# Kernel tuning notes

Hardware: AMD Instinct MI355X
Metric: run time of the kernel (lower is better)

## Reference

```python
import jax, jax.numpy as jnp
import numpy as np

B, L, E, H, FF = 2, 2048, 1024, 16, 4096
DH = E // H
EPS = 1e-5
# NOTE: source has attn_scale = 1 / dh**(-0.5) == sqrt(dh) (multiplies, not divides)
ATTN_SCALE = float(DH) ** 0.5


def _layernorm(x, w, b):
    mu = jnp.mean(x, axis=-1, keepdims=True)
    var = jnp.mean((x - mu) ** 2, axis=-1, keepdims=True)
    return (x - mu) * jax.lax.rsqrt(var + EPS) * w + b


def setup_inputs() -> dict:
    key = jax.random.key(0)
    ks = jax.random.split(key, 8)
    s = 0.02
    return {
        "x": jax.random.normal(ks[0], (B, L, E), jnp.float32),
        "ln1_w": jnp.ones((E,), jnp.float32),
        "ln1_b": jnp.zeros((E,), jnp.float32),
        "wq": jax.random.normal(ks[1], (E, E), jnp.float32) * s,
        "bq": jnp.zeros((E,), jnp.float32),
        "wk": jax.random.normal(ks[2], (E, E), jnp.float32) * s,
        "bk": jnp.zeros((E,), jnp.float32),
        "wv": jax.random.normal(ks[3], (E, E), jnp.float32) * s,
        "bv": jnp.zeros((E,), jnp.float32),
        "wo": jax.random.normal(ks[4], (E, E), jnp.float32) * s,
        "bo": jnp.zeros((E,), jnp.float32),
        "ln2_w": jnp.ones((E,), jnp.float32),
        "ln2_b": jnp.zeros((E,), jnp.float32),
        "wu": jax.random.normal(ks[5], (E, FF), jnp.float32) * s,
        "bu": jnp.zeros((FF,), jnp.float32),
        "wd": jax.random.normal(ks[6], (FF, E), jnp.float32) * s,
        "bd": jnp.zeros((E,), jnp.float32),
    }


def reference(x, ln1_w, ln1_b, wq, bq, wk, bk, wv, bv, wo, bo,
              ln2_w, ln2_b, wu, bu, wd, bd):
    # --- attention block (pre-LN, manual softmax attention) ---
    xn = _layernorm(x, ln1_w, ln1_b)                       # [B,L,E]
    q = (xn @ wq + bq).reshape(B, L, H, DH)
    k = (xn @ wk + bk).reshape(B, L, H, DH)
    v = (xn @ wv + bv).reshape(B, L, H, DH)
    score = jnp.einsum("blhd,bmhd->bhlm", q, k) * ATTN_SCALE  # [B,H,L,L]
    attn = jax.nn.softmax(score, axis=-1)
    ctx = jnp.einsum("bhlm,bmhd->blhd", attn, v).reshape(B, L, E)
    hidden = x + (ctx @ wo + bo)
    # --- FFN block (pre-LN, GELU) ---
    hn = _layernorm(hidden, ln2_w, ln2_b)
    up = jax.nn.gelu(hn @ wu + bu, approximate=False)      # [B,L,F]
    down = up @ wd + bd
    return hidden + down
```

## Files before the change

### kernel.cpp

```cpp
#include <hip/hip_runtime.h>
#include <stdint.h>


typedef __attribute__((ext_vector_type(8))) short short8;
typedef __attribute__((ext_vector_type(4))) float floatx4;
typedef __attribute__((ext_vector_type(16))) float floatx16;

extern "C" __device__ float __ocml_native_exp2_f32(float);
#define EXP2(x) __ocml_native_exp2_f32(x)

#define MFMA_BF16(a, b, c) __builtin_amdgcn_mfma_f32_16x16x32_bf16((a), (b), (c), 0, 0, 0)
#define MFMA32(a, b, c) __builtin_amdgcn_mfma_f32_32x32x16_bf16((a), (b), (c), 0, 0, 0)

__device__ __forceinline__ unsigned short f2bf(float f) {
  union { float f; unsigned int u; } v; v.f = f;
  unsigned int r = v.u + 0x7FFFu + ((v.u >> 16) & 1u);
  return (unsigned short)(r >> 16);
}

__device__ __forceinline__ unsigned int f2u(float f) {
  union { float f; unsigned int u; } v; v.f = f; return v.u;
}

__device__ __forceinline__ short8 pack4(unsigned a, unsigned b, unsigned c, unsigned d) {
  union { unsigned u[4]; short8 s; } v;
  v.u[0] = a; v.u[1] = b; v.u[2] = c; v.u[3] = d;
  return v.s;
}

__device__ __forceinline__ void gl_lds16(const unsigned short* g, unsigned short* l) {
  __builtin_amdgcn_global_load_lds(
      (const __attribute__((address_space(1))) unsigned int*)g,
      (__attribute__((address_space(3))) unsigned int*)l, 16, 0, 0);
}

template <int MODE, int BN>
__global__ __launch_bounds__(256)
void gemm_bt(const unsigned short* __restrict__ A,
             const unsigned short* __restrict__ Bt,
             const float* __restrict__ bias,
             void* __restrict__ outp,
             const float* __restrict__ res,
             int K,
             void* __restrict__ out2, void* __restrict__ out3,
             const float* __restrict__ bias2, const float* __restrict__ bias3) {
  constexpr int BM = 128, BK = 64;
  constexpr int MI = (BN == 128) ? 4 : 2;
  constexpr int NI = 4;
  __shared__ __align__(16) unsigned short As[BM * BK];
  __shared__ __align__(16) unsigned short Bs[BN * BK];
  const int tid = threadIdx.x;
  const int wave = tid >> 6, lane = tid & 63, l16 = lane & 15, quad = lane >> 4;
  const int m0 = blockIdx.y * BM, n0 = blockIdx.x * BN;
  const int wm = (BN == 128) ? (wave >> 1) * 64 : wave * 32;
  const int wn = (BN == 128) ? (wave & 1) * 64 : 0;
  const int sw = l16 & 7;
  const int sl0 = (quad ^ sw) << 3;
  const int sl1 = sl0 ^ 32;

  floatx4 acc[MI][NI] = {};

  for (int k0 = 0; k0 < K; k0 += BK) {
    __syncthreads();
#pragma unroll
    for (int c = 0; c < (BM * BK) / 2048; ++c) {
      const int e = (c * 256 + tid) * 8;
      const int row = e >> 6, c8 = (e >> 3) & 7;
      gl_lds16(A + (size_t)(m0 + row) * K + k0 + ((c8 ^ (row & 7)) << 3), &As[e]);
    }
#pragma unroll
    for (int c = 0; c < (BN * BK) / 2048; ++c) {
      const int e = (c * 256 + tid) * 8;
      const int row = e >> 6, c8 = (e >> 3) & 7;
      gl_lds16(Bt + (size_t)(n0 + row) * K + k0 + ((c8 ^ (row & 7)) << 3), &Bs[e]);
    }
    __syncthreads();

    short8 af0[MI], af1[MI], bf0[NI], bf1[NI];
#pragma unroll
    for (int i = 0; i < MI; ++i) {
      af0[i] = *(const short8*)&As[(wm + i * 16 + l16) * BK + sl0];
      af1[i] = *(const short8*)&As[(wm + i * 16 + l16) * BK + sl1];
    }
#pragma unroll
    for (int i = 0; i < NI; ++i) {
      bf0[i] = *(const short8*)&Bs[(wn + i * 16 + l16) * BK + sl0];
      bf1[i] = *(const short8*)&Bs[(wn + i * 16 + l16) * BK + sl1];
    }
    __builtin_amdgcn_sched_barrier(0);
#pragma unroll
    for (int mi = 0; mi < MI; ++mi)
#pragma unroll
      for (int ni = 0; ni < NI; ++ni) {
        acc[mi][ni] = MFMA_BF16(af0[mi], bf0[ni], acc[mi][ni]);
        acc[mi][ni] = MFMA_BF16(af1[mi], bf1[ni], acc[mi][ni]);
      }
  }

  const int seg = (MODE == 0) ? (n0 >> 10) : 0;
  const float* bptr = bias;
  if constexpr (MODE == 0) bptr = (seg == 0) ? bias : (seg == 1 ? bias2 : bias3);

  float bcol[NI];
#pragma unroll
  for (int ni = 0; ni < NI; ++ni) {
    const int n = n0 + wn + ni * 16 + l16;
    bcol[ni] = bptr[(MODE == 0) ? (n & 1023) : n];
  }

#pragma unroll
  for (int mi = 0; mi < MI; ++mi) {
#pragma unroll
    for (int r = 0; r < 4; ++r) {
      const int m = m0 + wm + mi * 16 + quad * 4 + r;
#pragma unroll
      for (int ni = 0; ni < NI; ++ni) {
        const int n = n0 + wn + ni * 16 + l16;
        const float c = acc[mi][ni][r] + bcol[ni];
        if constexpr (MODE == 0) {
          const int b_ = m >> 11, l = m & 2047, hd = n & 1023;
          const size_t idx =
              ((size_t)((b_ * 16 + (hd >> 6)) * 2048 + l)) * 64 + (hd & 63);
          if (seg == 0)       ((unsigned short*)outp)[idx] = f2bf(c * 11.5415603270f);
          else if (seg == 1)  ((unsigned short*)out2)[idx] = f2bf(c);
          else                ((unsigned short*)out3)[idx] = f2bf(c);
        } else if constexpr (MODE == 1) {
          ((float*)outp)[(size_t)m * 1024 + n] = res[(size_t)m * 1024 + n] + c;
        } else if constexpr (MODE == 2) {
          const float g = 0.5f * c * (1.0f + erff(c * 0.70710678118654752f));
          ((unsigned short*)outp)[(size_t)m * 4096 + n] = f2bf(g);
        } else {
          ((float*)outp)[(size_t)m * 1024 + n] = res[(size_t)m * 1024 + n] + c;
        }
      }
    }
  }
}

__device__ __forceinline__ void stage_p3(const unsigned short* __restrict__ A,
                                         const unsigned short* __restrict__ Bt,
                                         int K, int m0, int n0, int k0, int tid,
                                         unsigned short* Asb, unsigned short* Bsb) {
#pragma unroll
  for (int c = 0; c < 4; ++c) {
    const int e = (c * 256 + tid) * 8;
    const int row = e >> 6, c8 = (e >> 3) & 7;
    gl_lds16(A + (size_t)(m0 + row) * K + k0 + ((c8 ^ (row & 7)) << 3), Asb + e);
  }
#pragma unroll
  for (int c = 0; c < 2; ++c) {
    const int e = (c * 256 + tid) * 8;
    const int row = e >> 6, c8 = (e >> 3) & 7;
    gl_lds16(Bt + (size_t)(n0 + row) * K + k0 + ((c8 ^ (row & 7)) << 3), Bsb + e);
  }
}

__global__ __launch_bounds__(256)
void gemm_bt_p3(const unsigned short* __restrict__ A,
                const unsigned short* __restrict__ Bt,
                const float* __restrict__ bias,
                float* __restrict__ outp,
                const float* __restrict__ res,
                int K) {
  constexpr int BM = 128, BN = 64, BK = 64, MI = 2, NI = 4;
  __shared__ __align__(16) unsigned short As[3][BM * BK];
  __shared__ __align__(16) unsigned short Bs[3][BN * BK];
  const int tid = threadIdx.x;
  const int wave = tid >> 6, lane = tid & 63, l16 = lane & 15, quad = lane >> 4;
  const int m0 = blockIdx.y * BM, n0 = blockIdx.x * BN;
  const int wm = wave * 32;
  const int sw = l16 & 7;
  const int sl0 = (quad ^ sw) << 3;
  const int sl1 = sl0 ^ 32;

  floatx4 acc[MI][NI] = {};

  const int nt = K / BK;
  stage_p3(A, Bt, K, m0, n0, 0 * BK, tid, As[0], Bs[0]);
  stage_p3(A, Bt, K, m0, n0, 1 * BK, tid, As[1], Bs[1]);
  stage_p3(A, Bt, K, m0, n0, 2 * BK, tid, As[2], Bs[2]);

  for (int t = 0; t < nt; ++t) {
    if (t < nt - 2)       asm volatile("s_waitcnt vmcnt(12)" ::: "memory");
    else if (t == nt - 2) asm volatile("s_waitcnt vmcnt(6)" ::: "memory");
    else                  asm volatile("s_waitcnt vmcnt(0)" ::: "memory");
    __builtin_amdgcn_s_barrier();

    const unsigned short* Ab = As[t % 3];
    const unsigned short* Bb = Bs[t % 3];
    short8 af0[MI], af1[MI], bf0[NI], bf1[NI];
#pragma unroll
    for (int i = 0; i < MI; ++i) {
      af0[i] = *(const short8*)&Ab[(wm + i * 16 + l16) * BK + sl0];
      af1[i] = *(const short8*)&Ab[(wm + i * 16 + l16) * BK + sl1];
    }
#pragma unroll
    for (int i = 0; i < NI; ++i) {
      bf0[i] = *(const short8*)&Bb[(i * 16 + l16) * BK + sl0];
      bf1[i] = *(const short8*)&Bb[(i * 16 + l16) * BK + sl1];
    }
#pragma unroll
    for (int mi = 0; mi < MI; ++mi)
#pragma unroll
      for (int ni = 0; ni < NI; ++ni) {
        acc[mi][ni] = MFMA_BF16(af0[mi], bf0[ni], acc[mi][ni]);
        acc[mi][ni] = MFMA_BF16(af1[mi], bf1[ni], acc[mi][ni]);
      }

    __builtin_amdgcn_s_barrier();
    if (t + 3 < nt)
      stage_p3(A, Bt, K, m0, n0, (t + 3) * BK, tid, As[t % 3], Bs[t % 3]);
  }

  float bcol[NI];
#pragma unroll
  for (int ni = 0; ni < NI; ++ni) bcol[ni] = bias[n0 + ni * 16 + l16];

#pragma unroll
  for (int mi = 0; mi < MI; ++mi) {
#pragma unroll
    for (int r = 0; r < 4; ++r) {
      const int m = m0 + wm + mi * 16 + quad * 4 + r;
#pragma unroll
      for (int ni = 0; ni < NI; ++ni) {
        const int n = n0 + ni * 16 + l16;
        const float c = acc[mi][ni][r] + bcol[ni];
        outp[(size_t)m * 1024 + n] = res[(size_t)m * 1024 + n] + c;
      }
    }
  }
}

__global__ __launch_bounds__(256)
void layernorm_kernel(const float* __restrict__ x, const float* __restrict__ w,
                      const float* __restrict__ b, unsigned short* __restrict__ out) {
  const int row = blockIdx.x, tid = threadIdx.x;
  const int wave = tid >> 6, lane = tid & 63;
  const float4 v = ((const float4*)(x + (size_t)row * 1024))[tid];
  float s = v.x + v.y + v.z + v.w;
  float s2 = v.x * v.x + v.y * v.y + v.z * v.z + v.w * v.w;
#pragma unroll
  for (int off = 32; off > 0; off >>= 1) {
    s += __shfl_down(s, off);
    s2 += __shfl_down(s2, off);
  }
  __shared__ float red[8];
  if (lane == 0) { red[wave] = s; red[4 + wave] = s2; }
  __syncthreads();
  const float ts = red[0] + red[1] + red[2] + red[3];
  const float ts2 = red[4] + red[5] + red[6] + red[7];
  const float mu = ts * (1.0f / 1024.0f);
  const float var = ts2 * (1.0f / 1024.0f) - mu * mu;
  const float rs = rsqrtf(var + 1e-5f);
  const float4 wv = ((const float4*)w)[tid];
  const float4 bv = ((const float4*)b)[tid];
  ushort4 o;
  o.x = f2bf((v.x - mu) * rs * wv.x + bv.x);
  o.y = f2bf((v.y - mu) * rs * wv.y + bv.y);
  o.z = f2bf((v.z - mu) * rs * wv.z + bv.z);
  o.w = f2bf((v.w - mu) * rs * wv.w + bv.w);
  ((ushort4*)(out + (size_t)row * 1024))[tid] = o;
}

__global__ __launch_bounds__(256)
void transpose_cast4(const float* __restrict__ s0, const float* __restrict__ s1,
                     const float* __restrict__ s2, const float* __restrict__ s3,
                     unsigned short* __restrict__ dst) {
  __shared__ float tile[32][33];
  const int z = blockIdx.z;
  const float* in = (z == 0) ? s0 : (z == 1) ? s1 : (z == 2) ? s2 : s3;
  unsigned short* out = dst + (size_t)z * 1024 * 1024;
  const int tx = threadIdx.x, ty = threadIdx.y;
  const int c0 = blockIdx.x * 32, r0 = blockIdx.y * 32;
#pragma unroll
  for (int i = 0; i < 4; ++i)
    tile[ty + 8 * i][tx] = in[(size_t)(r0 + ty + 8 * i) * 1024 + c0 + tx];
  __syncthreads();
#pragma unroll
  for (int i = 0; i < 4; ++i)
    out[(size_t)(c0 + ty + 8 * i) * 1024 + r0 + tx] = f2bf(tile[tx][ty + 8 * i]);
}

__global__ __launch_bounds__(256)
void transpose_cast(const float* __restrict__ in, unsigned short* __restrict__ out,
                    int R, int C) {
  __shared__ float tile[32][33];
  const int tx = threadIdx.x, ty = threadIdx.y;
  const int c0 = blockIdx.x * 32, r0 = blockIdx.y * 32;
#pragma unroll
  for (int i = 0; i < 4; ++i)
    tile[ty + 8 * i][tx] = in[(size_t)(r0 + ty + 8 * i) * C + c0 + tx];
  __syncthreads();
#pragma unroll
  for (int i = 0; i < 4; ++i)
    out[(size_t)(c0 + ty + 8 * i) * R + r0 + tx] = f2bf(tile[tx][ty + 8 * i]);
}

__global__ __launch_bounds__(256)
void transpose_bf16(const unsigned short* __restrict__ in,
                    unsigned short* __restrict__ out, int R, int C) {
  __shared__ unsigned short tile[32][33];
  const size_t hoff = (size_t)blockIdx.z * R * C;
  in += hoff; out += hoff;
  const int tx = threadIdx.x, ty = threadIdx.y;
  const int c0 = blockIdx.x * 32, r0 = blockIdx.y * 32;
#pragma unroll
  for (int i = 0; i < 4; ++i)
    tile[ty + 8 * i][tx] = in[(size_t)(r0 + ty + 8 * i) * C + c0 + tx];
  __syncthreads();
  const int txp = (tx & ~12) | ((tx & 4) << 1) | ((tx & 8) >> 1);
#pragma unroll
  for (int i = 0; i < 4; ++i)
    out[(size_t)(c0 + ty + 8 * i) * R + r0 + txp] = tile[tx][ty + 8 * i];
}

__global__ __launch_bounds__(256, 4)
void flash_attn(const unsigned short* __restrict__ q,
                const unsigned short* __restrict__ k,
                const unsigned short* __restrict__ v,
                unsigned short* __restrict__ ctx) {
  __shared__ __align__(16) unsigned short Ks[2][64 * 64];
  __shared__ __align__(16) unsigned short Vs[2][64 * 64];
  const int bid = blockIdx.x + (blockIdx.y << 5);
  const int wg = (bid & 7) * 128 + (bid >> 3);
  const int bh = wg >> 5, qt = wg & 31;
  const int tid = threadIdx.x, wave = tid >> 6, lane = tid & 63;
  const int qw = wave & 1, kw = wave >> 1;
  const int lo = lane & 31, hi = lane >> 5, sw7 = lo & 7;
  const unsigned short* kb = k + (size_t)bh * 2048 * 64;
  const unsigned short* vb = v + (size_t)bh * 64 * 2048;

  const int qrow = qt * 64 + qw * 32 + lo;
  const unsigned short* qp = q + ((size_t)bh * 2048 + qrow) * 64;
  short8 qf[4];
#pragma unroll
  for (int kq = 0; kq < 4; ++kq) qf[kq] = *(const short8*)(qp + kq * 16 + hi * 8);

  int co[4];
#pragma unroll
  for (int j = 0; j < 4; ++j) co[j] = ((j * 2 + hi) ^ sw7) << 3;

  floatx16 O0 = {}, O1 = {};
  float m_run = -1e30f, l_run = 0.f;

  auto stage = [&](int t, int bufi) {
    const int kv0 = t * 64;
#pragma unroll
    for (int c = 0; c < 2; ++c) {
      const int e = (c * 256 + tid) * 8;
      const int r = e >> 6, ch = (e >> 3) & 7;
      const int sc = ((ch ^ (r & 7)) << 3);
      gl_lds16(kb + (size_t)(kv0 + r) * 64 + sc, &Ks[bufi][e]);
      gl_lds16(vb + (size_t)r * 2048 + kv0 + sc, &Vs[bufi][e]);
    }
  };
  stage(0, 0);

  for (int t = 0; t < 32; ++t) {
    __syncthreads();
    const int bufi = t & 1;
    if (t + 1 < 32) stage(t + 1, bufi ^ 1);

    const unsigned short* Kb = &Ks[bufi][0];
    const unsigned short* Vb = &Vs[bufi][0];

    floatx16 st = {};
    __builtin_amdgcn_s_setprio(1);
#pragma unroll
    for (int kq = 0; kq < 4; ++kq) {
      const short8 kf = *(const short8*)&Kb[(kw * 32 + lo) * 64 + co[kq]];
      st = MFMA32(kf, qf[kq], st);
    }
    __builtin_amdgcn_s_setprio(0);

    float mp[4];
#pragma unroll
    for (int r = 0; r < 4; ++r)
      mp[r] = fmaxf(fmaxf(st[r], st[r + 4]), fmaxf(st[r + 8], st[r + 12]));
    float mx = fmaxf(fmaxf(mp[0], mp[1]), fmaxf(mp[2], mp[3]));
    mx = fmaxf(mx, __shfl_xor(mx, 32));
    if (!__all(mx - m_run <= 8.0f)) {
      const float m_new = fmaxf(m_run, mx);
      const float alpha = EXP2(m_run - m_new);
      m_run = m_new;
      l_run *= alpha;
#pragma unroll
      for (int r = 0; r < 16; ++r) { O0[r] *= alpha; O1[r] *= alpha; }
    }
#pragma unroll
    for (int r = 0; r < 16; ++r) st[r] = EXP2(st[r] - m_run);
    float sp[4];
#pragma unroll
    for (int r = 0; r < 4; ++r)
      sp[r] = (st[r] + st[r + 4]) + (st[r + 8] + st[r + 12]);
    float rsum = (sp[0] + sp[1]) + (sp[2] + sp[3]);
    rsum += __shfl_xor(rsum, 32);
    l_run += rsum;

    unsigned pw[8];
#pragma unroll
    for (int i = 0; i < 8; ++i)
      pw[i] = __builtin_amdgcn_perm(f2u(st[2 * i + 1]), f2u(st[2 * i]), 0x07060302u);
    const short8 pf0 = pack4(pw[0], pw[1], pw[2], pw[3]);
    const short8 pf1 = pack4(pw[4], pw[5], pw[6], pw[7]);

    __builtin_amdgcn_s_setprio(1);
    {
      const short8 vf00 = *(const short8*)&Vb[lo * 64 + co[2 * kw]];
      const short8 vf01 = *(const short8*)&Vb[(32 + lo) * 64 + co[2 * kw]];
      O0 = MFMA32(vf00, pf0, O0);
      O1 = MFMA32(vf01, pf0, O1);
      const short8 vf10 = *(const short8*)&Vb[lo * 64 + co[2 * kw + 1]];
      const short8 vf11 = *(const short8*)&Vb[(32 + lo) * 64 + co[2 * kw + 1]];
      O0 = MFMA32(vf10, pf1, O0);
      O1 = MFMA32(vf11, pf1, O1);
    }
    __builtin_amdgcn_s_setprio(0);
  }

  __syncthreads();
  float* Os = (float*)&Ks[0][0];
  float* Ml = (float*)&Vs[0][0];
  if (kw == 1) {
    float* o = Os + (size_t)(qw * 64 + lane) * 32;
#pragma unroll
    for (int r = 0; r < 16; ++r) {
      o[(r + lane) & 31] = O0[r];
      o[(16 + r + lane) & 31] = O1[r];
    }
    Ml[qw * 64 + lane] = m_run;
    Ml[128 + qw * 64 + lane] = l_run;
  }
  __syncthreads();
  if (kw == 0) {
    const float m2 = Ml[qw * 64 + lane];
    const float l2 = Ml[128 + qw * 64 + lane];
    const float m = fmaxf(m_run, m2);
    const float a1 = EXP2(m_run - m), a2 = EXP2(m2 - m);
    const float linv = 1.0f / (l_run * a1 + l2 * a2);
    const float* o = Os + (size_t)(qw * 64 + lane) * 32;
    float f0[16], f1[16];
#pragma unroll
    for (int r = 0; r < 16; ++r) {
      f0[r] = (O0[r] * a1 + o[(r + lane) & 31] * a2) * linv;
      f1[r] = (O1[r] * a1 + o[(16 + r + lane) & 31] * a2) * linv;
    }
    const int b_ = bh >> 4, h_ = bh & 15;
    unsigned short* op = ctx + ((size_t)(b_ * 2048) + qrow) * 1024 + h_ * 64;
#pragma unroll
    for (int rq = 0; rq < 4; ++rq) {
      ushort4 a4, b4;
      a4.x = f2bf(f0[rq * 4 + 0]); a4.y = f2bf(f0[rq * 4 + 1]);
      a4.z = f2bf(f0[rq * 4 + 2]); a4.w = f2bf(f0[rq * 4 + 3]);
      *(ushort4*)(op + rq * 8 + hi * 4) = a4;
      b4.x = f2bf(f1[rq * 4 + 0]); b4.y = f2bf(f1[rq * 4 + 1]);
      b4.z = f2bf(f1[rq * 4 + 2]); b4.w = f2bf(f1[rq * 4 + 3]);
      *(ushort4*)(op + 32 + rq * 8 + hi * 4) = b4;
    }
  }
}

extern "C" void kernel_launch(void* const* d_in, const int* in_sizes, int n_in,
                              void* d_out, int out_size, void* d_ws, size_t ws_size,
                              hipStream_t stream) {
  const float* x     = (const float*)d_in[0];
  const float* ln1_w = (const float*)d_in[1];
  const float* ln1_b = (const float*)d_in[2];
  const float* wq    = (const float*)d_in[3];
  const float* bq    = (const float*)d_in[4];
  const float* wk    = (const float*)d_in[5];
  const float* bk    = (const float*)d_in[6];
  const float* wv    = (const float*)d_in[7];
  const float* bv    = (const float*)d_in[8];
  const float* wo    = (const float*)d_in[9];
  const float* bo    = (const float*)d_in[10];
  const float* ln2_w = (const float*)d_in[11];
  const float* ln2_b = (const float*)d_in[12];
  const float* wu    = (const float*)d_in[13];
  const float* bu    = (const float*)d_in[14];
  const float* wd    = (const float*)d_in[15];
  const float* bd    = (const float*)d_in[16];

  char* W = (char*)d_ws;
  const size_t MB = 1ull << 20;
  unsigned short* wqkvT = (unsigned short*)(W + 0 * MB);
  unsigned short* woT   = (unsigned short*)(W + 6 * MB);
  unsigned short* wuT   = (unsigned short*)(W + 8 * MB);
  unsigned short* wdT   = (unsigned short*)(W + 16 * MB);
  unsigned short* xn    = (unsigned short*)(W + 24 * MB);
  unsigned short* qb    = (unsigned short*)(W + 32 * MB);
  unsigned short* kb    = (unsigned short*)(W + 40 * MB);
  unsigned short* vb    = (unsigned short*)(W + 48 * MB);
  unsigned short* cx    = (unsigned short*)(W + 56 * MB);
  float*          hid   = (float*)(W + 64 * MB);
  unsigned short* up    = (unsigned short*)(W + 24 * MB);

  const dim3 tb(32, 8);
  transpose_cast4<<<dim3(32, 32, 4), tb, 0, stream>>>(wq, wk, wv, wo, wqkvT);
  transpose_cast<<<dim3(128, 32), tb, 0, stream>>>(wu, wuT, 1024, 4096);
  transpose_cast<<<dim3(32, 128), tb, 0, stream>>>(wd, wdT, 4096, 1024);

  layernorm_kernel<<<4096, 256, 0, stream>>>(x, ln1_w, ln1_b, xn);
  gemm_bt<0, 128><<<dim3(24, 32), 256, 0, stream>>>(
      xn, wqkvT, bq, qb, nullptr, 1024, kb, cx, bk, bv);
  transpose_bf16<<<dim3(2, 64, 32), tb, 0, stream>>>(cx, vb, 2048, 64);
  flash_attn<<<dim3(32, 32), 256, 0, stream>>>(qb, kb, vb, cx);
  gemm_bt_p3<<<dim3(16, 32), 256, 0, stream>>>(
      cx, woT, bo, hid, x, 1024);

  layernorm_kernel<<<4096, 256, 0, stream>>>(hid, ln2_w, ln2_b, cx);
  gemm_bt<2, 128><<<dim3(32, 32), 256, 0, stream>>>(
      cx, wuT, bu, up, nullptr, 1024, nullptr, nullptr, nullptr, nullptr);
  gemm_bt_p3<<<dim3(16, 32), 256, 0, stream>>>(
      up, wdT, bd, (float*)d_out, hid, 4096);
}
```

Before: 375.9 us.

## Double-buffer LDS tiles in QKV and up-projection GEMMs with async prefetch

Replaces the single-buffered gemm_bt with gemm_bt_2b, which keeps two LDS stages and prefetches tile t+2 while computing tile t. It uses explicit vmcnt waits and raw s_barrier calls instead of two __syncthreads per K step. The goal is to hide global-to-LDS load latency behind MFMA work in the QKV and FFN-up GEMMs. In exchange, LDS use doubles to 64KB per block, which may lower occupancy.

```diff
diff --git a/kernel.cpp b/kernel.cpp
--- a/kernel.cpp
+++ b/kernel.cpp
@@ -34,58 +34,70 @@
       (__attribute__((address_space(3))) unsigned int*)l, 16, 0, 0);
 }
 
-template <int MODE, int BN>
+__device__ __forceinline__ void stage_2b(const unsigned short* __restrict__ A,
+                                         const unsigned short* __restrict__ Bt,
+                                         int K, int m0, int n0, int k0, int tid,
+                                         unsigned short* Asb, unsigned short* Bsb) {
+#pragma unroll
+  for (int c = 0; c < 4; ++c) {
+    const int e = (c * 256 + tid) * 8;
+    const int row = e >> 6, c8 = (e >> 3) & 7;
+    gl_lds16(A + (size_t)(m0 + row) * K + k0 + ((c8 ^ (row & 7)) << 3), Asb + e);
+  }
+#pragma unroll
+  for (int c = 0; c < 4; ++c) {
+    const int e = (c * 256 + tid) * 8;
+    const int row = e >> 6, c8 = (e >> 3) & 7;
+    gl_lds16(Bt + (size_t)(n0 + row) * K + k0 + ((c8 ^ (row & 7)) << 3), Bsb + e);
+  }
+}
+
+template <int MODE>
 __global__ __launch_bounds__(256)
-void gemm_bt(const unsigned short* __restrict__ A,
-             const unsigned short* __restrict__ Bt,
-             const float* __restrict__ bias,
-             void* __restrict__ outp,
-             const float* __restrict__ res,
-             int K,
-             void* __restrict__ out2, void* __restrict__ out3,
-             const float* __restrict__ bias2, const float* __restrict__ bias3) {
-  constexpr int BM = 128, BK = 64;
-  constexpr int MI = (BN == 128) ? 4 : 2;
-  constexpr int NI = 4;
-  __shared__ __align__(16) unsigned short As[BM * BK];
-  __shared__ __align__(16) unsigned short Bs[BN * BK];
+void gemm_bt_2b(const unsigned short* __restrict__ A,
+                const unsigned short* __restrict__ Bt,
+                const float* __restrict__ bias,
+                void* __restrict__ outp,
+                const float* __restrict__ res,
+                int K,
+                void* __restrict__ out2, void* __restrict__ out3,
+                const float* __restrict__ bias2, const float* __restrict__ bias3) {
+  constexpr int BM = 128, BN = 128, BK = 64;
+  constexpr int MI = 4, NI = 4;
+  __shared__ __align__(16) unsigned short As[2][BM * BK];
+  __shared__ __align__(16) unsigned short Bs[2][BN * BK];
   const int tid = threadIdx.x;
   const int wave = tid >> 6, lane = tid & 63, l16 = lane & 15, quad = lane >> 4;
   const int m0 = blockIdx.y * BM, n0 = blockIdx.x * BN;
-  const int wm = (BN == 128) ? (wave >> 1) * 64 : wave * 32;
-  const int wn = (BN == 128) ? (wave & 1) * 64 : 0;
+  const int wm = (wave >> 1) * 64;
+  const int wn = (wave & 1) * 64;
   const int sw = l16 & 7;
   const int sl0 = (quad ^ sw) << 3;
   const int sl1 = sl0 ^ 32;
 
   floatx4 acc[MI][NI] = {};
 
-  for (int k0 = 0; k0 < K; k0 += BK) {
-    __syncthreads();
-#pragma unroll
-    for (int c = 0; c < (BM * BK) / 2048; ++c) {
-      const int e = (c * 256 + tid) * 8;
-      const int row = e >> 6, c8 = (e >> 3) & 7;
-      gl_lds16(A + (size_t)(m0 + row) * K + k0 + ((c8 ^ (row & 7)) << 3), &As[e]);
-    }
-#pragma unroll
-    for (int c = 0; c < (BN * BK) / 2048; ++c) {
-      const int e = (c * 256 + tid) * 8;
-      const int row = e >> 6, c8 = (e >> 3) & 7;
-      gl_lds16(Bt + (size_t)(n0 + row) * K + k0 + ((c8 ^ (row & 7)) << 3), &Bs[e]);
-    }
-    __syncthreads();
-
+  const int nt = K / BK;
+  stage_2b(A, Bt, K, m0, n0, 0 * BK, tid, As[0], Bs[0]);
+  stage_2b(A, Bt, K, m0, n0, 1 * BK, tid, As[1], Bs[1]);
+
+  for (int t = 0; t < nt; ++t) {
+    if (t < nt - 1) asm volatile("s_waitcnt vmcnt(8)" ::: "memory");
+    else            asm volatile("s_waitcnt vmcnt(0)" ::: "memory");
+    __builtin_amdgcn_s_barrier();
+
+    const unsigned short* Ab = As[t & 1];
+    const unsigned short* Bb = Bs[t & 1];
     short8 af0[MI], af1[MI], bf0[NI], bf1[NI];
 #pragma unroll
     for (int i = 0; i < MI; ++i) {
-      af0[i] = *(const short8*)&As[(wm + i * 16 + l16) * BK + sl0];
-      af1[i] = *(const short8*)&As[(wm + i * 16 + l16) * BK + sl1];
+      af0[i] = *(const short8*)&Ab[(wm + i * 16 + l16) * BK + sl0];
+      af1[i] = *(const short8*)&Ab[(wm + i * 16 + l16) * BK + sl1];
     }
 #pragma unroll
     for (int i = 0; i < NI; ++i) {
-      bf0[i] = *(const short8*)&Bs[(wn + i * 16 + l16) * BK + sl0];
-      bf1[i] = *(const short8*)&Bs[(wn + i * 16 + l16) * BK + sl1];
+      bf0[i] = *(const short8*)&Bb[(wn + i * 16 + l16) * BK + sl0];
+      bf1[i] = *(const short8*)&Bb[(wn + i * 16 + l16) * BK + sl1];
     }
     __builtin_amdgcn_sched_barrier(0);
 #pragma unroll
@@ -95,6 +107,10 @@
         acc[mi][ni] = MFMA_BF16(af0[mi], bf0[ni], acc[mi][ni]);
         acc[mi][ni] = MFMA_BF16(af1[mi], bf1[ni], acc[mi][ni]);
       }
+
+    __builtin_amdgcn_s_barrier();
+    if (t + 2 < nt)
+      stage_2b(A, Bt, K, m0, n0, (t + 2) * BK, tid, As[t & 1], Bs[t & 1]);
   }
 
   const int seg = (MODE == 0) ? (n0 >> 10) : 0;
@@ -124,13 +140,9 @@
           if (seg == 0)       ((unsigned short*)outp)[idx] = f2bf(c * 11.5415603270f);
           else if (seg == 1)  ((unsigned short*)out2)[idx] = f2bf(c);
           else                ((unsigned short*)out3)[idx] = f2bf(c);
-        } else if constexpr (MODE == 1) {
-          ((float*)outp)[(size_t)m * 1024 + n] = res[(size_t)m * 1024 + n] + c;
-        } else if constexpr (MODE == 2) {
+        } else {
           const float g = 0.5f * c * (1.0f + erff(c * 0.70710678118654752f));
           ((unsigned short*)outp)[(size_t)m * 4096 + n] = f2bf(g);
-        } else {
-          ((float*)outp)[(size_t)m * 1024 + n] = res[(size_t)m * 1024 + n] + c;
         }
       }
     }
@@ -501,7 +513,7 @@
   transpose_cast<<<dim3(32, 128), tb, 0, stream>>>(wd, wdT, 4096, 1024);
 
   layernorm_kernel<<<4096, 256, 0, stream>>>(x, ln1_w, ln1_b, xn);
-  gemm_bt<0, 128><<<dim3(24, 32), 256, 0, stream>>>(
+  gemm_bt_2b<0><<<dim3(24, 32), 256, 0, stream>>>(
       xn, wqkvT, bq, qb, nullptr, 1024, kb, cx, bk, bv);
   transpose_bf16<<<dim3(2, 64, 32), tb, 0, stream>>>(cx, vb, 2048, 64);
   flash_attn<<<dim3(32, 32), 256, 0, stream>>>(qb, kb, vb, cx);
@@ -509,7 +521,7 @@
       cx, woT, bo, hid, x, 1024);
 
   layernorm_kernel<<<4096, 256, 0, stream>>>(hid, ln2_w, ln2_b, cx);
-  gemm_bt<2, 128><<<dim3(32, 32), 256, 0, stream>>>(
+  gemm_bt_2b<2><<<dim3(32, 32), 256, 0, stream>>>(
       cx, wuT, bu, up, nullptr, 1024, nullptr, nullptr, nullptr, nullptr);
   gemm_bt_p3<<<dim3(16, 32), 256, 0, stream>>>(
       up, wdT, bd, (float*)d_out, hid, 4096);
```

Measured after the change: 380.7 us (median of 3 runs). About the same (+1.3%).
